# Optimization experiments

Measured on AMD Instinct MI355X. Metric: run time of the kernel, lower is better.

## Reference

```python
import jax, jax.numpy as jnp
import numpy as np

B, S, D = 64, 2048, 64

def setup_inputs() -> dict:
    key = jax.random.key(0)
    k1, k2, k3, k4 = jax.random.split(key, 4)
    query = jax.random.normal(k1, (B, S, D), dtype=jnp.float32)
    keyt = jax.random.normal(k2, (B, S, D), dtype=jnp.float32)
    value = jax.random.normal(k3, (B, S, D), dtype=jnp.float32)
    mask = jax.random.randint(k4, (1, S, S), 0, 2, dtype=jnp.int32)
    return {"query": query, "key": keyt, "value": value, "mask": mask}

def reference(query, key, value, mask):
    # scores: [B, S, S]
    scale = jnp.sqrt(jnp.asarray(value.shape[-1], dtype=query.dtype))
    scores = jnp.einsum('bqd,bkd->bqk', query, key) / scale
    scores = jnp.where(mask == 0, jnp.asarray(-1e9, dtype=scores.dtype), scores)
    attention_weights = jax.nn.softmax(scores, axis=-1)
    # dropout p=0.0 -> identity
    context = jnp.einsum('bqk,bkd->bqd', attention_weights, value)
    return (context, attention_weights)
```

## Files before the change

### kernel.cpp

```cpp
#include <hip/hip_runtime.h>

#define NB 64
#define NS 2048
#define ND 64
#define KSTEP 64
#define NIT (NS / KSTEP)

typedef __bf16 bf16x8 __attribute__((ext_vector_type(8)));
typedef float f32x4 __attribute__((ext_vector_type(4)));
typedef unsigned int u32;
typedef u32 u32x2 __attribute__((ext_vector_type(2)));
typedef u32 u32x4 __attribute__((ext_vector_type(4)));
typedef unsigned short u16;
typedef u16 u16x8 __attribute__((ext_vector_type(8)));

#define C2F 0.18033688011112042f

__device__ __forceinline__ float fexp2(float x) {
#if __has_builtin(__builtin_amdgcn_exp2f)
  return __builtin_amdgcn_exp2f(x);
#else
  return exp2f(x);
#endif
}
__device__ __forceinline__ float flog2(float x) {
#if __has_builtin(__builtin_amdgcn_logf)
  return __builtin_amdgcn_logf(x);
#else
  return log2f(x);
#endif
}

#define TILE_BARRIER()                                   \
  do {                                                   \
    asm volatile("s_waitcnt lgkmcnt(0)" ::: "memory");   \
    __builtin_amdgcn_s_barrier();                        \
    asm volatile("" ::: "memory");                       \
  } while (0)

__device__ __forceinline__ u16 f2bs(float x) {
  __bf16 h = (__bf16)x;
  return __builtin_bit_cast(u16, h);
}

__device__ __forceinline__ bf16x8 cvt8(f32x4 a, f32x4 b) {
  bf16x8 r;
  r[0] = (__bf16)a[0]; r[1] = (__bf16)a[1]; r[2] = (__bf16)a[2]; r[3] = (__bf16)a[3];
  r[4] = (__bf16)b[0]; r[5] = (__bf16)b[1]; r[6] = (__bf16)b[2]; r[7] = (__bf16)b[3];
  return r;
}

__global__ __launch_bounds__(256) void prep_cast_k(const float* __restrict__ K,
                                                   u16* __restrict__ Kbf) {
  const size_t i = ((size_t)blockIdx.x * 256 + threadIdx.x) * 8;
  f32x4 a = __builtin_nontemporal_load((const f32x4*)(K + i));
  f32x4 b = __builtin_nontemporal_load((const f32x4*)(K + i + 4));
  *(bf16x8*)(Kbf + i) = cvt8(a, b);
}

__global__ __launch_bounds__(256) void prep_transp_v(const float* __restrict__ V,
                                                     u16* __restrict__ VT) {
  __shared__ __attribute__((aligned(16))) u16 T[64][72];
  const int b = blockIdx.x >> 5, kt = blockIdx.x & 31;
  const float* src = V + ((size_t)b * NS + kt * 64) * ND;
  {
    const int k = threadIdx.x >> 2, d0 = (threadIdx.x & 3) * 16;
    const float* p = src + (size_t)k * ND + d0;
    f32x4 a0 = __builtin_nontemporal_load((const f32x4*)p);
    f32x4 a1 = __builtin_nontemporal_load((const f32x4*)(p + 4));
    f32x4 a2 = __builtin_nontemporal_load((const f32x4*)(p + 8));
    f32x4 a3 = __builtin_nontemporal_load((const f32x4*)(p + 12));
    *(bf16x8*)&T[k][d0]     = cvt8(a0, a1);
    *(bf16x8*)&T[k][d0 + 8] = cvt8(a2, a3);
  }
  __syncthreads();
  const int d = threadIdx.x >> 2, k0 = (threadIdx.x & 3) * 16;
  u16x8 r0, r1;
#pragma unroll
  for (int j = 0; j < 8; ++j) {
    const int P0 = k0 + j, P1 = k0 + 8 + j;
    const int s0 = 32 * (P0 >> 5) + 16 * ((P0 >> 2) & 1) + 4 * ((P0 >> 3) & 3) + (P0 & 3);
    const int s1 = 32 * (P1 >> 5) + 16 * ((P1 >> 2) & 1) + 4 * ((P1 >> 3) & 3) + (P1 & 3);
    r0[j] = T[s0][d];
    r1[j] = T[s1][d];
  }
  u16* dst = VT + ((size_t)b * ND + d) * NS + kt * 64 + k0;
  *(u16x8*)dst = r0;
  *(u16x8*)(dst + 8) = r1;
}

__global__ __launch_bounds__(256) void prep_pack_mask(const int* __restrict__ M,
                                                      unsigned long long* __restrict__ Mb) {
  const size_t i = (size_t)blockIdx.x * 256 + threadIdx.x;
  const unsigned long long bal = __ballot(M[i] != 0);
  if ((threadIdx.x & 63) == 0) Mb[i >> 6] = bal;
}

template <bool PRE>
__global__ __launch_bounds__(512, 3) void DotProductAttention_22436909154804_kernel(
    const float* __restrict__ Q, const float* __restrict__ K,
    const float* __restrict__ V, const int* __restrict__ M,
    const u16* __restrict__ Kbf, const u16* __restrict__ VTbf,
    const u32* __restrict__ Mb, float* __restrict__ ctx, float* __restrict__ wts) {
  __shared__ __attribute__((aligned(16))) u16 Kt[2][64][72];
  __shared__ __attribute__((aligned(16))) u16 Vt[2][64][72];
  __shared__ float Rs[2][64];

  const int tid  = threadIdx.x;
  const int lane = tid & 63;
  const int w    = tid >> 6;
  const int wq   = w & 3;
  const int kt   = w >> 2;
  const int g    = lane >> 4;
  const int c    = lane & 15;

  const int bid = blockIdx.x;
  const int vb  = (bid & 7) * 256 + (bid >> 3);
  const int b   = vb >> 5;
  const int qt  = vb & 31;
  const int q0w = qt * 64 + wq * 16;
  const size_t bq = (size_t)b * NS;

  const float* qp = Q + (bq + q0w + c) * ND + 8 * g;
  f32x4 qa = __builtin_nontemporal_load((const f32x4*)qp);
  f32x4 qb = __builtin_nontemporal_load((const f32x4*)(qp + 4));
  const bf16x8 qf0 = cvt8(qa, qb);
  qa = __builtin_nontemporal_load((const f32x4*)(qp + 32));
  qb = __builtin_nontemporal_load((const f32x4*)(qp + 36));
  const bf16x8 qf1 = cvt8(qa, qb);

  const u16* Kbb = PRE ? (Kbf + bq * ND) : (const u16*)nullptr;
  const u16* VTb = PRE ? (VTbf + bq * ND) : (const u16*)nullptr;
  const float* Kb32 = K + bq * ND;
  const float* Vb32 = V + bq * ND;
  const int* Mr   = M + (size_t)(q0w + c) * NS + kt * 32;
  const u32* MbRow = Mb + (size_t)(q0w + c) * (NS / 32);
  const u32* Mbr   = MbRow + kt;

  const bool isK = tid < 256;
  const int st   = tid & 255;

  auto msel = [](float e, u32 mm, int idx) -> float {
    u32 keep = (u32)(((int)(mm << (31 - idx))) >> 31);
    return __uint_as_float(__float_as_uint(e) & keep);
  };

  const f32x4 zz = {0.f, 0.f, 0.f, 0.f};
  float rs = 0.f;

  if (PRE) {
    const int r1  = tid >> 2;
    const int cc1 = (tid & 3) * 16;
    u16x8 pa, pb;
    auto issueP1 = [&](int kb) {
      const u16* p = Kbb + (size_t)(kb + r1) * ND + cc1;
      pa = *(const u16x8*)p;
      pb = *(const u16x8*)(p + 8);
    };
    auto writeP1 = [&](int pair) {
      u16(*dst)[72] = pair ? Vt[r1 >> 6] : Kt[r1 >> 6];
      *(u16x8*)&dst[r1 & 63][cc1]     = pa;
      *(u16x8*)&dst[r1 & 63][cc1 + 8] = pb;
    };
    issueP1(0);
    writeP1(0);
    __syncthreads();
    for (int it = 0; it < 16; ++it) {
      const int pair = it & 1;
      if (it + 1 < 16) issueP1((it + 1) * 128);
      const u32x2 mv = *(const u32x2*)(MbRow + it * 4 + kt * 2);
      u16(*B)[72] = pair ? Vt[kt] : Kt[kt];
#pragma unroll
      for (int j = 0; j < 4; ++j) {
        bf16x8 a0 = *(const bf16x8*)&B[16 * j + c][8 * g];
        bf16x8 a1 = *(const bf16x8*)&B[16 * j + c][32 + 8 * g];
        f32x4 s = __builtin_amdgcn_mfma_f32_16x16x32_bf16(a0, qf0, zz, 0, 0, 0);
        s = __builtin_amdgcn_mfma_f32_16x16x32_bf16(a1, qf1, s, 0, 0, 0);
        const u32 mm = (j < 2) ? mv.x : mv.y;
        const int base = 16 * (j & 1) + 4 * g;
        rs += msel(fexp2(s[0] * C2F), mm, base + 0)
            + msel(fexp2(s[1] * C2F), mm, base + 1)
            + msel(fexp2(s[2] * C2F), mm, base + 2)
            + msel(fexp2(s[3] * C2F), mm, base + 3);
      }
      if (it + 1 < 16) writeP1((it + 1) & 1);
      TILE_BARRIER();
    }
  } else {
    f32x4 kf0, kf1, kf2, kf3;
    auto issueK1 = [&](int kb) {
      if (isK) {
        const int r = st >> 2, cc = (st & 3) * 16;
        const float* p = Kb32 + (size_t)(kb + r) * ND + cc;
        kf0 = *(const f32x4*)p;       kf1 = *(const f32x4*)(p + 4);
        kf2 = *(const f32x4*)(p + 8); kf3 = *(const f32x4*)(p + 12);
      }
    };
    auto writeK1 = [&](int buf) {
      if (isK) {
        const int r = st >> 2, cc = (st & 3) * 16;
        *(bf16x8*)&Kt[buf][r][cc]     = cvt8(kf0, kf1);
        *(bf16x8*)&Kt[buf][r][cc + 8] = cvt8(kf2, kf3);
      }
    };
    issueK1(0);
    writeK1(0);
    __syncthreads();
    for (int it = 0; it < NIT; ++it) {
      const int cur = it & 1, kb = it * KSTEP;
      if (it + 1 < NIT) issueK1(kb + KSTEP);
#pragma unroll
      for (int j = 0; j < 2; ++j) {
        bf16x8 a0 = *(const bf16x8*)&Kt[cur][kt * 32 + 16 * j + c][8 * g];
        bf16x8 a1 = *(const bf16x8*)&Kt[cur][kt * 32 + 16 * j + c][32 + 8 * g];
        f32x4 s = __builtin_amdgcn_mfma_f32_16x16x32_bf16(a0, qf0, zz, 0, 0, 0);
        s = __builtin_amdgcn_mfma_f32_16x16x32_bf16(a1, qf1, s, 0, 0, 0);
        const int4 m4 = *(const int4*)(Mr + kb + 16 * j + 4 * g);
        rs += (m4.x ? fexp2(s[0] * C2F) : 0.f)
            + (m4.y ? fexp2(s[1] * C2F) : 0.f)
            + (m4.z ? fexp2(s[2] * C2F) : 0.f)
            + (m4.w ? fexp2(s[3] * C2F) : 0.f);
      }
      if (it + 1 < NIT) writeK1((it + 1) & 1);
      TILE_BARRIER();
    }
  }
  rs += __shfl_xor(rs, 16);
  rs += __shfl_xor(rs, 32);

  u16x8 sp0, sp1;
  f32x4 kf0, kf1, kf2, kf3;
  auto issueKV = [&](int kb) {
    if (PRE) {
      if (isK) {
        const int r = st >> 2, cc = (st & 3) * 16;
        const u16* p = Kbb + (size_t)(kb + r) * ND + cc;
        sp0 = *(const u16x8*)p; sp1 = *(const u16x8*)(p + 8);
      } else {
        const int d = st >> 2, kc = (st & 3) * 16;
        const u16* p = VTb + (size_t)d * NS + kb + kc;
        sp0 = *(const u16x8*)p; sp1 = *(const u16x8*)(p + 8);
      }
    } else {
      if (isK) {
        const int r = st >> 2, cc = (st & 3) * 16;
        const float* p = Kb32 + (size_t)(kb + r) * ND + cc;
        kf0 = *(const f32x4*)p;       kf1 = *(const f32x4*)(p + 4);
        kf2 = *(const f32x4*)(p + 8); kf3 = *(const f32x4*)(p + 12);
      } else {
        const int k = st >> 2, d0 = (st & 3) * 16;
        const float* p = Vb32 + (size_t)(kb + k) * ND + d0;
        kf0 = *(const f32x4*)p;       kf1 = *(const f32x4*)(p + 4);
        kf2 = *(const f32x4*)(p + 8); kf3 = *(const f32x4*)(p + 12);
      }
    }
  };
  auto writeKV = [&](int buf) {
    if (PRE) {
      if (isK) {
        const int r = st >> 2, cc = (st & 3) * 16;
        *(u16x8*)&Kt[buf][r][cc] = sp0; *(u16x8*)&Kt[buf][r][cc + 8] = sp1;
      } else {
        const int d = st >> 2, kc = (st & 3) * 16;
        *(u16x8*)&Vt[buf][d][kc] = sp0; *(u16x8*)&Vt[buf][d][kc + 8] = sp1;
      }
    } else {
      if (isK) {
        const int r = st >> 2, cc = (st & 3) * 16;
        *(bf16x8*)&Kt[buf][r][cc]     = cvt8(kf0, kf1);
        *(bf16x8*)&Kt[buf][r][cc + 8] = cvt8(kf2, kf3);
      } else {
        const int k = st >> 2, d0 = (st & 3) * 16;
        bf16x8 v0 = cvt8(kf0, kf1), v1 = cvt8(kf2, kf3);
#pragma unroll
        for (int j = 0; j < 8; ++j) {
          Vt[buf][d0 + j][k]     = __builtin_bit_cast(u16, v0[j]);
          Vt[buf][d0 + 8 + j][k] = __builtin_bit_cast(u16, v1[j]);
        }
      }
    }
  };

  issueKV(0);
  if (lane < 16) Rs[kt][wq * 16 + c] = rs;
  __syncthreads();
  const float l2inv = -flog2(Rs[0][wq * 16 + c] + Rs[1][wq * 16 + c]);
  writeKV(0);
  __syncthreads();

  f32x4 acc[4] = {zz, zz, zz, zz};
  float* wrow = wts + (bq + q0w + c) * NS + kt * 32;
  for (int it = 0; it < NIT; ++it) {
    const int cur = it & 1, kb = it * KSTEP;
    if (it + 1 < NIT) issueKV(kb + KSTEP);
    u32 mm = 0;
    if (PRE) mm = Mbr[kb >> 5];

    u32 wpk[4];
#pragma unroll
    for (int j = 0; j < 2; ++j) {
      bf16x8 a0 = *(const bf16x8*)&Kt[cur][kt * 32 + 16 * j + c][8 * g];
      bf16x8 a1 = *(const bf16x8*)&Kt[cur][kt * 32 + 16 * j + c][32 + 8 * g];
      f32x4 s = __builtin_amdgcn_mfma_f32_16x16x32_bf16(a0, qf0, zz, 0, 0, 0);
      s = __builtin_amdgcn_mfma_f32_16x16x32_bf16(a1, qf1, s, 0, 0, 0);
      float w0, w1, w2, w3;
      if (PRE) {
        w0 = msel(fexp2(fmaf(s[0], C2F, l2inv)), mm, 16 * j + 4 * g + 0);
        w1 = msel(fexp2(fmaf(s[1], C2F, l2inv)), mm, 16 * j + 4 * g + 1);
        w2 = msel(fexp2(fmaf(s[2], C2F, l2inv)), mm, 16 * j + 4 * g + 2);
        w3 = msel(fexp2(fmaf(s[3], C2F, l2inv)), mm, 16 * j + 4 * g + 3);
      } else {
        const int4 m4 = *(const int4*)(Mr + kb + 16 * j + 4 * g);
        w0 = m4.x ? fexp2(fmaf(s[0], C2F, l2inv)) : 0.f;
        w1 = m4.y ? fexp2(fmaf(s[1], C2F, l2inv)) : 0.f;
        w2 = m4.z ? fexp2(fmaf(s[2], C2F, l2inv)) : 0.f;
        w3 = m4.w ? fexp2(fmaf(s[3], C2F, l2inv)) : 0.f;
      }
      f32x4 wv = {w0, w1, w2, w3};
      __builtin_nontemporal_store(wv, (f32x4*)(wrow + kb + 16 * j + 4 * g));
      wpk[2 * j]     = (u32)f2bs(w0) | ((u32)f2bs(w1) << 16);
      wpk[2 * j + 1] = (u32)f2bs(w2) | ((u32)f2bs(w3) << 16);
    }

    u32x4 wu = {wpk[0], wpk[1], wpk[2], wpk[3]};
    bf16x8 wb = __builtin_bit_cast(bf16x8, wu);
#pragma unroll
    for (int dt = 0; dt < 4; ++dt) {
      bf16x8 va;
      if (PRE) {
        va = *(const bf16x8*)&Vt[cur][dt * 16 + c][kt * 32 + 8 * g];
      } else {
        u32x2 vlo = *(const u32x2*)&Vt[cur][dt * 16 + c][kt * 32 + 4 * g];
        u32x2 vhi = *(const u32x2*)&Vt[cur][dt * 16 + c][kt * 32 + 16 + 4 * g];
        u32x4 vau = {vlo.x, vlo.y, vhi.x, vhi.y};
        va = __builtin_bit_cast(bf16x8, vau);
      }
      acc[dt] = __builtin_amdgcn_mfma_f32_16x16x32_bf16(va, wb, acc[dt], 0, 0, 0);
    }

    if (it + 1 < NIT) writeKV((it + 1) & 1);
    TILE_BARRIER();
  }

  float* red = (float*)&Kt[0][0][0] + wq * 1088;
  if (kt == 1) {
#pragma unroll
    for (int dt = 0; dt < 4; ++dt)
      *(f32x4*)&red[c * 68 + dt * 16 + 4 * g] = acc[dt];
  }
  __syncthreads();
  if (kt == 0) {
    float* crow = ctx + (bq + q0w + c) * ND;
#pragma unroll
    for (int dt = 0; dt < 4; ++dt) {
      f32x4 vv = acc[dt] + *(const f32x4*)&red[c * 68 + dt * 16 + 4 * g];
      __builtin_nontemporal_store(vv, (f32x4*)(crow + dt * 16 + 4 * g));
    }
  }
}

extern "C" void kernel_launch(void* const* d_in, const int* in_sizes, int n_in,
                              void* d_out, int out_size, void* d_ws, size_t ws_size,
                              hipStream_t stream) {
  const float* Q = (const float*)d_in[0];
  const float* K = (const float*)d_in[1];
  const float* V = (const float*)d_in[2];
  const int*   M = (const int*)d_in[3];
  float* ctx = (float*)d_out;
  float* wts = (float*)d_out + (size_t)NB * NS * ND;

  dim3 grid(NB * (NS / 64));
  dim3 block(512);

  constexpr size_t KBF_B = (size_t)NB * NS * ND * 2;
  constexpr size_t MB_B  = (size_t)NS * NS / 8;
  u16* Kbf = (u16*)d_ws;
  u16* VTb = (u16*)((char*)d_ws + KBF_B);
  unsigned long long* Mb64 = (unsigned long long*)((char*)d_ws + 2 * KBF_B);

  if (ws_size >= 2 * KBF_B + MB_B) {
    hipLaunchKernelGGL(prep_cast_k, dim3(NB * NS * ND / 8 / 256), dim3(256), 0, stream, K, Kbf);
    hipLaunchKernelGGL(prep_transp_v, dim3(NB * (NS / 64)), dim3(256), 0, stream, V, VTb);
    hipLaunchKernelGGL(prep_pack_mask, dim3(NS * NS / 256), dim3(256), 0, stream, M, Mb64);
    hipLaunchKernelGGL(DotProductAttention_22436909154804_kernel<true>, grid, block, 0, stream,
                       Q, K, V, M, Kbf, VTb, (const u32*)Mb64, ctx, wts);
  } else {
    hipLaunchKernelGGL(DotProductAttention_22436909154804_kernel<false>, grid, block, 0, stream,
                       Q, K, V, M, (const u16*)nullptr, (const u16*)nullptr,
                       (const u32*)nullptr, ctx, wts);
  }
}
```

Before: 336.1 us.

## Switch attention kernel to 32x32x16 MFMA with 4-wave blocks

Replaces the 16x16x32 bf16 MFMA tiling with 32x32x16 MFMAs, so each wave handles 32 query rows, and cuts blocks from 8 waves to 4 (launch bounds 256,4). Fragment layouts, mask bit indexing, the V transpose permutation (now a swap23 helper) and the cross-wave reduction are reworked to match the new accumulator layout. The aim is fewer MFMA issues and LDS fragment reads per output element. The cost is more registers per wave and fewer waves per block to hide latency. fexp2 also switches from the amdgcn builtin to exp2f, which may add range-handling instructions.

New measurement: 766.7 us. +128.1%, slower.

```diff
diff --git a/kernel.cpp b/kernel.cpp
--- a/kernel.cpp
+++ b/kernel.cpp
@@ -8,6 +8,7 @@
 
 typedef __bf16 bf16x8 __attribute__((ext_vector_type(8)));
 typedef float f32x4 __attribute__((ext_vector_type(4)));
+typedef float f32x16 __attribute__((ext_vector_type(16)));
 typedef unsigned int u32;
 typedef u32 u32x2 __attribute__((ext_vector_type(2)));
 typedef u32 u32x4 __attribute__((ext_vector_type(4)));
@@ -16,20 +17,8 @@
 
 #define C2F 0.18033688011112042f
 
-__device__ __forceinline__ float fexp2(float x) {
-#if __has_builtin(__builtin_amdgcn_exp2f)
-  return __builtin_amdgcn_exp2f(x);
-#else
-  return exp2f(x);
-#endif
-}
-__device__ __forceinline__ float flog2(float x) {
-#if __has_builtin(__builtin_amdgcn_logf)
-  return __builtin_amdgcn_logf(x);
-#else
-  return log2f(x);
-#endif
-}
+__device__ __forceinline__ float fexp2(float x) { return exp2f(x); }
+__device__ __forceinline__ float flog2(float x) { return log2f(x); }
 
 #define TILE_BARRIER()                                   \
   do {                                                   \
@@ -48,6 +37,10 @@
   r[0] = (__bf16)a[0]; r[1] = (__bf16)a[1]; r[2] = (__bf16)a[2]; r[3] = (__bf16)a[3];
   r[4] = (__bf16)b[0]; r[5] = (__bf16)b[1]; r[6] = (__bf16)b[2]; r[7] = (__bf16)b[3];
   return r;
+}
+
+__device__ __host__ __forceinline__ int swap23(int p) {
+  return (p & ~12) | ((p & 4) << 1) | ((p & 8) >> 1);
 }
 
 __global__ __launch_bounds__(256) void prep_cast_k(const float* __restrict__ K,
@@ -78,11 +71,8 @@
   u16x8 r0, r1;
 #pragma unroll
   for (int j = 0; j < 8; ++j) {
-    const int P0 = k0 + j, P1 = k0 + 8 + j;
-    const int s0 = 32 * (P0 >> 5) + 16 * ((P0 >> 2) & 1) + 4 * ((P0 >> 3) & 3) + (P0 & 3);
-    const int s1 = 32 * (P1 >> 5) + 16 * ((P1 >> 2) & 1) + 4 * ((P1 >> 3) & 3) + (P1 & 3);
-    r0[j] = T[s0][d];
-    r1[j] = T[s1][d];
+    r0[j] = T[swap23(k0 + j)][d];
+    r1[j] = T[swap23(k0 + 8 + j)][d];
   }
   u16* dst = VT + ((size_t)b * ND + d) * NS + kt * 64 + k0;
   *(u16x8*)dst = r0;
@@ -97,7 +87,7 @@
 }
 
 template <bool PRE>
-__global__ __launch_bounds__(512, 3) void DotProductAttention_22436909154804_kernel(
+__global__ __launch_bounds__(256, 4) void DotProductAttention_22436909154804_kernel(
     const float* __restrict__ Q, const float* __restrict__ K,
     const float* __restrict__ V, const int* __restrict__ M,
     const u16* __restrict__ Kbf, const u16* __restrict__ VTbf,
@@ -109,58 +99,56 @@
   const int tid  = threadIdx.x;
   const int lane = tid & 63;
   const int w    = tid >> 6;
-  const int wq   = w & 3;
-  const int kt   = w >> 2;
-  const int g    = lane >> 4;
-  const int c    = lane & 15;
+  const int wq   = w & 1;
+  const int kt   = w >> 1;
+  const int q    = lane & 31;
+  const int h    = lane >> 5;
 
   const int bid = blockIdx.x;
   const int vb  = (bid & 7) * 256 + (bid >> 3);
   const int b   = vb >> 5;
   const int qt  = vb & 31;
-  const int q0w = qt * 64 + wq * 16;
+  const int q0w = qt * 64 + wq * 32;
   const size_t bq = (size_t)b * NS;
 
-  const float* qp = Q + (bq + q0w + c) * ND + 8 * g;
-  f32x4 qa = __builtin_nontemporal_load((const f32x4*)qp);
-  f32x4 qb = __builtin_nontemporal_load((const f32x4*)(qp + 4));
-  const bf16x8 qf0 = cvt8(qa, qb);
-  qa = __builtin_nontemporal_load((const f32x4*)(qp + 32));
-  qb = __builtin_nontemporal_load((const f32x4*)(qp + 36));
-  const bf16x8 qf1 = cvt8(qa, qb);
+  const float* qp = Q + (bq + q0w + q) * ND + 8 * h;
+  bf16x8 qf[4];
+#pragma unroll
+  for (int s = 0; s < 4; ++s) {
+    f32x4 qa = __builtin_nontemporal_load((const f32x4*)(qp + 16 * s));
+    f32x4 qb = __builtin_nontemporal_load((const f32x4*)(qp + 16 * s + 4));
+    qf[s] = cvt8(qa, qb);
+  }
 
   const u16* Kbb = PRE ? (Kbf + bq * ND) : (const u16*)nullptr;
   const u16* VTb = PRE ? (VTbf + bq * ND) : (const u16*)nullptr;
   const float* Kb32 = K + bq * ND;
   const float* Vb32 = V + bq * ND;
-  const int* Mr   = M + (size_t)(q0w + c) * NS + kt * 32;
-  const u32* MbRow = Mb + (size_t)(q0w + c) * (NS / 32);
-  const u32* Mbr   = MbRow + kt;
-
-  const bool isK = tid < 256;
-  const int st   = tid & 255;
+  const int* Mr32  = M + (size_t)(q0w + q) * NS + kt * 32;
+  const u32* MbRow = Mb + (size_t)(q0w + q) * (NS / 32);
 
   auto msel = [](float e, u32 mm, int idx) -> float {
     u32 keep = (u32)(((int)(mm << (31 - idx))) >> 31);
     return __uint_as_float(__float_as_uint(e) & keep);
   };
 
-  const f32x4 zz = {0.f, 0.f, 0.f, 0.f};
   float rs = 0.f;
 
   if (PRE) {
-    const int r1  = tid >> 2;
-    const int cc1 = (tid & 3) * 16;
-    u16x8 pa, pb;
+    const int r1  = tid >> 1;
+    const int cc1 = (tid & 1) * 32;
+    u16x8 pa0, pa1, pa2, pa3;
     auto issueP1 = [&](int kb) {
       const u16* p = Kbb + (size_t)(kb + r1) * ND + cc1;
-      pa = *(const u16x8*)p;
-      pb = *(const u16x8*)(p + 8);
+      pa0 = *(const u16x8*)p;        pa1 = *(const u16x8*)(p + 8);
+      pa2 = *(const u16x8*)(p + 16); pa3 = *(const u16x8*)(p + 24);
     };
     auto writeP1 = [&](int pair) {
       u16(*dst)[72] = pair ? Vt[r1 >> 6] : Kt[r1 >> 6];
-      *(u16x8*)&dst[r1 & 63][cc1]     = pa;
-      *(u16x8*)&dst[r1 & 63][cc1 + 8] = pb;
+      *(u16x8*)&dst[r1 & 63][cc1]      = pa0;
+      *(u16x8*)&dst[r1 & 63][cc1 + 8]  = pa1;
+      *(u16x8*)&dst[r1 & 63][cc1 + 16] = pa2;
+      *(u16x8*)&dst[r1 & 63][cc1 + 24] = pa3;
     };
     issueP1(0);
     writeP1(0);
@@ -171,17 +159,17 @@
       const u32x2 mv = *(const u32x2*)(MbRow + it * 4 + kt * 2);
       u16(*B)[72] = pair ? Vt[kt] : Kt[kt];
 #pragma unroll
-      for (int j = 0; j < 4; ++j) {
-        bf16x8 a0 = *(const bf16x8*)&B[16 * j + c][8 * g];
-        bf16x8 a1 = *(const bf16x8*)&B[16 * j + c][32 + 8 * g];
-        f32x4 s = __builtin_amdgcn_mfma_f32_16x16x32_bf16(a0, qf0, zz, 0, 0, 0);
-        s = __builtin_amdgcn_mfma_f32_16x16x32_bf16(a1, qf1, s, 0, 0, 0);
-        const u32 mm = (j < 2) ? mv.x : mv.y;
-        const int base = 16 * (j & 1) + 4 * g;
-        rs += msel(fexp2(s[0] * C2F), mm, base + 0)
-            + msel(fexp2(s[1] * C2F), mm, base + 1)
-            + msel(fexp2(s[2] * C2F), mm, base + 2)
-            + msel(fexp2(s[3] * C2F), mm, base + 3);
+      for (int win = 0; win < 2; ++win) {
+        f32x16 s = {};
+#pragma unroll
+        for (int slab = 0; slab < 4; ++slab) {
+          bf16x8 a = *(const bf16x8*)&B[win * 32 + q][16 * slab + 8 * h];
+          s = __builtin_amdgcn_mfma_f32_32x32x16_bf16(a, qf[slab], s, 0, 0, 0);
+        }
+        const u32 mm = win ? mv.y : mv.x;
+#pragma unroll
+        for (int e = 0; e < 16; ++e)
+          rs += msel(fexp2(s[e] * C2F), mm, 4 * h + (e & 3) + 8 * (e >> 2));
       }
       if (it + 1 < 16) writeP1((it + 1) & 1);
       TILE_BARRIER();
@@ -189,19 +177,15 @@
   } else {
     f32x4 kf0, kf1, kf2, kf3;
     auto issueK1 = [&](int kb) {
-      if (isK) {
-        const int r = st >> 2, cc = (st & 3) * 16;
-        const float* p = Kb32 + (size_t)(kb + r) * ND + cc;
-        kf0 = *(const f32x4*)p;       kf1 = *(const f32x4*)(p + 4);
-        kf2 = *(const f32x4*)(p + 8); kf3 = *(const f32x4*)(p + 12);
-      }
+      const int r = tid >> 2, cc = (tid & 3) * 16;
+      const float* p = Kb32 + (size_t)(kb + r) * ND + cc;
+      kf0 = *(const f32x4*)p;       kf1 = *(const f32x4*)(p + 4);
+      kf2 = *(const f32x4*)(p + 8); kf3 = *(const f32x4*)(p + 12);
     };
     auto writeK1 = [&](int buf) {
-      if (isK) {
-        const int r = st >> 2, cc = (st & 3) * 16;
-        *(bf16x8*)&Kt[buf][r][cc]     = cvt8(kf0, kf1);
-        *(bf16x8*)&Kt[buf][r][cc + 8] = cvt8(kf2, kf3);
-      }
+      const int r = tid >> 2, cc = (tid & 3) * 16;
+      *(bf16x8*)&Kt[buf][r][cc]     = cvt8(kf0, kf1);
+      *(bf16x8*)&Kt[buf][r][cc + 8] = cvt8(kf2, kf3);
     };
     issueK1(0);
     writeK1(0);
@@ -209,152 +193,160 @@
     for (int it = 0; it < NIT; ++it) {
       const int cur = it & 1, kb = it * KSTEP;
       if (it + 1 < NIT) issueK1(kb + KSTEP);
-#pragma unroll
-      for (int j = 0; j < 2; ++j) {
-        bf16x8 a0 = *(const bf16x8*)&Kt[cur][kt * 32 + 16 * j + c][8 * g];
-        bf16x8 a1 = *(const bf16x8*)&Kt[cur][kt * 32 + 16 * j + c][32 + 8 * g];
-        f32x4 s = __builtin_amdgcn_mfma_f32_16x16x32_bf16(a0, qf0, zz, 0, 0, 0);
-        s = __builtin_amdgcn_mfma_f32_16x16x32_bf16(a1, qf1, s, 0, 0, 0);
-        const int4 m4 = *(const int4*)(Mr + kb + 16 * j + 4 * g);
-        rs += (m4.x ? fexp2(s[0] * C2F) : 0.f)
-            + (m4.y ? fexp2(s[1] * C2F) : 0.f)
-            + (m4.z ? fexp2(s[2] * C2F) : 0.f)
-            + (m4.w ? fexp2(s[3] * C2F) : 0.f);
+      f32x16 s = {};
+#pragma unroll
+      for (int slab = 0; slab < 4; ++slab) {
+        bf16x8 a = *(const bf16x8*)&Kt[cur][kt * 32 + q][16 * slab + 8 * h];
+        s = __builtin_amdgcn_mfma_f32_32x32x16_bf16(a, qf[slab], s, 0, 0, 0);
+      }
+#pragma unroll
+      for (int j = 0; j < 4; ++j) {
+        const int4 m4 = *(const int4*)(Mr32 + kb + 8 * j + 4 * h);
+        rs += (m4.x ? fexp2(s[4 * j + 0] * C2F) : 0.f)
+            + (m4.y ? fexp2(s[4 * j + 1] * C2F) : 0.f)
+            + (m4.z ? fexp2(s[4 * j + 2] * C2F) : 0.f)
+            + (m4.w ? fexp2(s[4 * j + 3] * C2F) : 0.f);
       }
       if (it + 1 < NIT) writeK1((it + 1) & 1);
       TILE_BARRIER();
     }
   }
-  rs += __shfl_xor(rs, 16);
   rs += __shfl_xor(rs, 32);
 
-  u16x8 sp0, sp1;
-  f32x4 kf0, kf1, kf2, kf3;
+  const bool isK = tid < 128;
+  const int t2   = tid & 127;
+  const int row2 = t2 >> 1;
+  const int cc2  = (t2 & 1) * 32;
+  u16x8 sp0, sp1, sp2, sp3;
+  f32x4 g0, g1, g2, g3, g4, g5, g6, g7;
+  const int vkp = (t2 & 31) * 2;
+  const int vdb = (t2 >> 5) * 16;
+  const int vpc = swap23(vkp);
+
   auto issueKV = [&](int kb) {
     if (PRE) {
-      if (isK) {
-        const int r = st >> 2, cc = (st & 3) * 16;
-        const u16* p = Kbb + (size_t)(kb + r) * ND + cc;
-        sp0 = *(const u16x8*)p; sp1 = *(const u16x8*)(p + 8);
-      } else {
-        const int d = st >> 2, kc = (st & 3) * 16;
-        const u16* p = VTb + (size_t)d * NS + kb + kc;
-        sp0 = *(const u16x8*)p; sp1 = *(const u16x8*)(p + 8);
-      }
+      const u16* p = isK ? (Kbb + (size_t)(kb + row2) * ND + cc2)
+                         : (VTb + (size_t)row2 * NS + kb + cc2);
+      sp0 = *(const u16x8*)p;        sp1 = *(const u16x8*)(p + 8);
+      sp2 = *(const u16x8*)(p + 16); sp3 = *(const u16x8*)(p + 24);
     } else {
       if (isK) {
-        const int r = st >> 2, cc = (st & 3) * 16;
-        const float* p = Kb32 + (size_t)(kb + r) * ND + cc;
-        kf0 = *(const f32x4*)p;       kf1 = *(const f32x4*)(p + 4);
-        kf2 = *(const f32x4*)(p + 8); kf3 = *(const f32x4*)(p + 12);
+        const float* p = Kb32 + (size_t)(kb + row2) * ND + cc2;
+        g0 = *(const f32x4*)p;        g1 = *(const f32x4*)(p + 4);
+        g2 = *(const f32x4*)(p + 8);  g3 = *(const f32x4*)(p + 12);
+        g4 = *(const f32x4*)(p + 16); g5 = *(const f32x4*)(p + 20);
+        g6 = *(const f32x4*)(p + 24); g7 = *(const f32x4*)(p + 28);
       } else {
-        const int k = st >> 2, d0 = (st & 3) * 16;
-        const float* p = Vb32 + (size_t)(kb + k) * ND + d0;
-        kf0 = *(const f32x4*)p;       kf1 = *(const f32x4*)(p + 4);
-        kf2 = *(const f32x4*)(p + 8); kf3 = *(const f32x4*)(p + 12);
+        const float* p = Vb32 + (size_t)(kb + vkp) * ND + vdb;
+        g0 = *(const f32x4*)p;        g1 = *(const f32x4*)(p + 4);
+        g2 = *(const f32x4*)(p + 8);  g3 = *(const f32x4*)(p + 12);
+        g4 = *(const f32x4*)(p + ND);      g5 = *(const f32x4*)(p + ND + 4);
+        g6 = *(const f32x4*)(p + ND + 8);  g7 = *(const f32x4*)(p + ND + 12);
       }
     }
   };
   auto writeKV = [&](int buf) {
     if (PRE) {
-      if (isK) {
-        const int r = st >> 2, cc = (st & 3) * 16;
-        *(u16x8*)&Kt[buf][r][cc] = sp0; *(u16x8*)&Kt[buf][r][cc + 8] = sp1;
-      } else {
-        const int d = st >> 2, kc = (st & 3) * 16;
-        *(u16x8*)&Vt[buf][d][kc] = sp0; *(u16x8*)&Vt[buf][d][kc + 8] = sp1;
-      }
+      u16(*dst)[72] = isK ? Kt[buf] : Vt[buf];
+      *(u16x8*)&dst[row2][cc2]      = sp0;
+      *(u16x8*)&dst[row2][cc2 + 8]  = sp1;
+      *(u16x8*)&dst[row2][cc2 + 16] = sp2;
+      *(u16x8*)&dst[row2][cc2 + 24] = sp3;
     } else {
       if (isK) {
-        const int r = st >> 2, cc = (st & 3) * 16;
-        *(bf16x8*)&Kt[buf][r][cc]     = cvt8(kf0, kf1);
-        *(bf16x8*)&Kt[buf][r][cc + 8] = cvt8(kf2, kf3);
+        *(bf16x8*)&Kt[buf][row2][cc2]      = cvt8(g0, g1);
+        *(bf16x8*)&Kt[buf][row2][cc2 + 8]  = cvt8(g2, g3);
+        *(bf16x8*)&Kt[buf][row2][cc2 + 16] = cvt8(g4, g5);
+        *(bf16x8*)&Kt[buf][row2][cc2 + 24] = cvt8(g6, g7);
       } else {
-        const int k = st >> 2, d0 = (st & 3) * 16;
-        bf16x8 v0 = cvt8(kf0, kf1), v1 = cvt8(kf2, kf3);
-#pragma unroll
-        for (int j = 0; j < 8; ++j) {
-          Vt[buf][d0 + j][k]     = __builtin_bit_cast(u16, v0[j]);
-          Vt[buf][d0 + 8 + j][k] = __builtin_bit_cast(u16, v1[j]);
-        }
+        const f32x4 lo[4] = {g0, g1, g2, g3}, hi[4] = {g4, g5, g6, g7};
+#pragma unroll
+        for (int j = 0; j < 16; ++j)
+          *(u32*)&Vt[buf][vdb + j][vpc] =
+              (u32)f2bs(lo[j >> 2][j & 3]) | ((u32)f2bs(hi[j >> 2][j & 3]) << 16);
       }
     }
   };
 
   issueKV(0);
-  if (lane < 16) Rs[kt][wq * 16 + c] = rs;
+  if (lane < 32) Rs[kt][wq * 32 + q] = rs;
   __syncthreads();
-  const float l2inv = -flog2(Rs[0][wq * 16 + c] + Rs[1][wq * 16 + c]);
+  const float l2inv = -flog2(Rs[0][wq * 32 + q] + Rs[1][wq * 32 + q]);
   writeKV(0);
   __syncthreads();
 
-  f32x4 acc[4] = {zz, zz, zz, zz};
-  float* wrow = wts + (bq + q0w + c) * NS + kt * 32;
+  f32x16 acc0 = {}, acc1 = {};
+  float* wrow = wts + (bq + q0w + q) * NS + kt * 32;
   for (int it = 0; it < NIT; ++it) {
     const int cur = it & 1, kb = it * KSTEP;
     if (it + 1 < NIT) issueKV(kb + KSTEP);
     u32 mm = 0;
-    if (PRE) mm = Mbr[kb >> 5];
-
-    u32 wpk[4];
-#pragma unroll
-    for (int j = 0; j < 2; ++j) {
-      bf16x8 a0 = *(const bf16x8*)&Kt[cur][kt * 32 + 16 * j + c][8 * g];
-      bf16x8 a1 = *(const bf16x8*)&Kt[cur][kt * 32 + 16 * j + c][32 + 8 * g];
-      f32x4 s = __builtin_amdgcn_mfma_f32_16x16x32_bf16(a0, qf0, zz, 0, 0, 0);
-      s = __builtin_amdgcn_mfma_f32_16x16x32_bf16(a1, qf1, s, 0, 0, 0);
+    if (PRE) mm = MbRow[it * 2 + kt];
+
+    f32x16 s = {};
+#pragma unroll
+    for (int slab = 0; slab < 4; ++slab) {
+      bf16x8 a = *(const bf16x8*)&Kt[cur][kt * 32 + q][16 * slab + 8 * h];
+      s = __builtin_amdgcn_mfma_f32_32x32x16_bf16(a, qf[slab], s, 0, 0, 0);
+    }
+
+    u32 wpk[8];
+#pragma unroll
+    for (int j = 0; j < 4; ++j) {
       float w0, w1, w2, w3;
       if (PRE) {
-        w0 = msel(fexp2(fmaf(s[0], C2F, l2inv)), mm, 16 * j + 4 * g + 0);
-        w1 = msel(fexp2(fmaf(s[1], C2F, l2inv)), mm, 16 * j + 4 * g + 1);
-        w2 = msel(fexp2(fmaf(s[2], C2F, l2inv)), mm, 16 * j + 4 * g + 2);
-        w3 = msel(fexp2(fmaf(s[3], C2F, l2inv)), mm, 16 * j + 4 * g + 3);
+        w0 = msel(fexp2(fmaf(s[4 * j + 0], C2F, l2inv)), mm, 4 * h + 8 * j + 0);
+        w1 = msel(fexp2(fmaf(s[4 * j + 1], C2F, l2inv)), mm, 4 * h + 8 * j + 1);
+        w2 = msel(fexp2(fmaf(s[4 * j + 2], C2F, l2inv)), mm, 4 * h + 8 * j + 2);
+        w3 = msel(fexp2(fmaf(s[4 * j + 3], C2F, l2inv)), mm, 4 * h + 8 * j + 3);
       } else {
-        const int4 m4 = *(const int4*)(Mr + kb + 16 * j + 4 * g);
-        w0 = m4.x ? fexp2(fmaf(s[0], C2F, l2inv)) : 0.f;
-        w1 = m4.y ? fexp2(fmaf(s[1], C2F, l2inv)) : 0.f;
-        w2 = m4.z ? fexp2(fmaf(s[2], C2F, l2inv)) : 0.f;
-        w3 = m4.w ? fexp2(fmaf(s[3], C2F, l2inv)) : 0.f;
+        const int4 m4 = *(const int4*)(Mr32 + kb + 8 * j + 4 * h);
+        w0 = m4.x ? fexp2(fmaf(s[4 * j + 0], C2F, l2inv)) : 0.f;
+        w1 = m4.y ? fexp2(fmaf(s[4 * j + 1], C2F, l2inv)) : 0.f;
+        w2 = m4.z ? fexp2(fmaf(s[4 * j + 2], C2F, l2inv)) : 0.f;
+        w3 = m4.w ? fexp2(fmaf(s[4 * j + 3], C2F, l2inv)) : 0.f;
       }
       f32x4 wv = {w0, w1, w2, w3};
-      __builtin_nontemporal_store(wv, (f32x4*)(wrow + kb + 16 * j + 4 * g));
+      __builtin_nontemporal_store(wv, (f32x4*)(wrow + kb + 8 * j + 4 * h));
       wpk[2 * j]     = (u32)f2bs(w0) | ((u32)f2bs(w1) << 16);
       wpk[2 * j + 1] = (u32)f2bs(w2) | ((u32)f2bs(w3) << 16);
     }
 
-    u32x4 wu = {wpk[0], wpk[1], wpk[2], wpk[3]};
-    bf16x8 wb = __builtin_bit_cast(bf16x8, wu);
-#pragma unroll
-    for (int dt = 0; dt < 4; ++dt) {
-      bf16x8 va;
-      if (PRE) {
-        va = *(const bf16x8*)&Vt[cur][dt * 16 + c][kt * 32 + 8 * g];
-      } else {
-        u32x2 vlo = *(const u32x2*)&Vt[cur][dt * 16 + c][kt * 32 + 4 * g];
-        u32x2 vhi = *(const u32x2*)&Vt[cur][dt * 16 + c][kt * 32 + 16 + 4 * g];
-        u32x4 vau = {vlo.x, vlo.y, vhi.x, vhi.y};
-        va = __builtin_bit_cast(bf16x8, vau);
-      }
-      acc[dt] = __builtin_amdgcn_mfma_f32_16x16x32_bf16(va, wb, acc[dt], 0, 0, 0);
+#pragma unroll
+    for (int sl = 0; sl < 2; ++sl) {
+      u32x4 wu = {wpk[4 * sl], wpk[4 * sl + 1], wpk[4 * sl + 2], wpk[4 * sl + 3]};
+      bf16x8 wb = __builtin_bit_cast(bf16x8, wu);
+      bf16x8 va0 = *(const bf16x8*)&Vt[cur][q][kt * 32 + sl * 16 + 8 * h];
+      acc0 = __builtin_amdgcn_mfma_f32_32x32x16_bf16(va0, wb, acc0, 0, 0, 0);
+      bf16x8 va1 = *(const bf16x8*)&Vt[cur][32 + q][kt * 32 + sl * 16 + 8 * h];
+      acc1 = __builtin_amdgcn_mfma_f32_32x32x16_bf16(va1, wb, acc1, 0, 0, 0);
     }
 
     if (it + 1 < NIT) writeKV((it + 1) & 1);
     TILE_BARRIER();
   }
 
-  float* red = (float*)&Kt[0][0][0] + wq * 1088;
+  float* red = (float*)&Kt[0][0][0] + wq * (32 * 68);
   if (kt == 1) {
 #pragma unroll
-    for (int dt = 0; dt < 4; ++dt)
-      *(f32x4*)&red[c * 68 + dt * 16 + 4 * g] = acc[dt];
+    for (int j = 0; j < 4; ++j) {
+      f32x4 v0 = {acc0[4 * j], acc0[4 * j + 1], acc0[4 * j + 2], acc0[4 * j + 3]};
+      f32x4 v1 = {acc1[4 * j], acc1[4 * j + 1], acc1[4 * j + 2], acc1[4 * j + 3]};
+      *(f32x4*)&red[q * 68 + 8 * j + 4 * h]      = v0;
+      *(f32x4*)&red[q * 68 + 32 + 8 * j + 4 * h] = v1;
+    }
   }
   __syncthreads();
   if (kt == 0) {
-    float* crow = ctx + (bq + q0w + c) * ND;
-#pragma unroll
-    for (int dt = 0; dt < 4; ++dt) {
-      f32x4 vv = acc[dt] + *(const f32x4*)&red[c * 68 + dt * 16 + 4 * g];
-      __builtin_nontemporal_store(vv, (f32x4*)(crow + dt * 16 + 4 * g));
+    float* crow = ctx + (bq + q0w + q) * ND;
+#pragma unroll
+    for (int j = 0; j < 4; ++j) {
+      f32x4 v0 = {acc0[4 * j], acc0[4 * j + 1], acc0[4 * j + 2], acc0[4 * j + 3]};
+      f32x4 v1 = {acc1[4 * j], acc1[4 * j + 1], acc1[4 * j + 2], acc1[4 * j + 3]};
+      v0 += *(const f32x4*)&red[q * 68 + 8 * j + 4 * h];
+      v1 += *(const f32x4*)&red[q * 68 + 32 + 8 * j + 4 * h];
+      __builtin_nontemporal_store(v0, (f32x4*)(crow + 8 * j + 4 * h));
+      __builtin_nontemporal_store(v1, (f32x4*)(crow + 32 + 8 * j + 4 * h));
     }
   }
 }
@@ -370,7 +362,7 @@
   float* wts = (float*)d_out + (size_t)NB * NS * ND;
 
   dim3 grid(NB * (NS / 64));
-  dim3 block(512);
+  dim3 block(256);
 
   constexpr size_t KBF_B = (size_t)NB * NS * ND * 2;
   constexpr size_t MB_B  = (size_t)NS * NS / 8;
```
